# Optimization experiments

Measured on AMD Instinct MI355X. Metric: run time of the kernel, lower is better.

The kernel has to match this reference:

```python
import jax, jax.numpy as jnp
import numpy as np

N_NODES = 100000
N_EDGES = 1600000
IN_DIM = 128
HIDDEN = 128
EPS = 1e-5  # BatchNorm1d default eps


def gcn_conv(x, src, dst, W, b, n_nodes):
    """PyG GCNConv with default add_self_loops=True, edge_weight=None.
    out = D^{-1/2} (A + I) D^{-1/2} X W + b, deg computed from dst (col)."""
    xw = x @ W  # [N, out_dim] -- transform before propagate, as in PyG
    ones = jnp.ones((src.shape[0],), dtype=x.dtype)
    deg = jax.ops.segment_sum(ones, dst, num_segments=n_nodes) + 1.0  # +1 self-loop
    dis = jax.lax.rsqrt(deg)  # deg >= 1 always
    norm = dis[src] * dis[dst]  # [E]
    msgs = xw[src] * norm[:, None]  # [E, out_dim] gather (irregular access)
    agg = jax.ops.segment_sum(msgs, dst, num_segments=n_nodes)
    agg = agg + xw * (1.0 / deg)[:, None]  # self-loop contribution, norm = 1/deg_i
    return agg + b


def batch_norm(x, gamma, beta):
    # training-mode BatchNorm1d: biased batch statistics over the node dim
    m = jnp.mean(x, axis=0)
    v = jnp.mean(jnp.square(x - m), axis=0)
    return gamma * (x - m) * jax.lax.rsqrt(v + EPS) + beta


def setup_inputs() -> dict:
    key = jax.random.key(0)
    ks = jax.random.split(key, 6)
    x = jax.random.normal(ks[0], (N_NODES, IN_DIM), dtype=jnp.float32)
    edge_index = jax.random.randint(ks[1], (2, N_EDGES), 0, N_NODES, dtype=jnp.int64)
    # Glorot-ish scaled weights
    W1 = jax.random.normal(ks[2], (IN_DIM, HIDDEN), dtype=jnp.float32) / np.sqrt(IN_DIM)
    W2 = jax.random.normal(ks[3], (HIDDEN, HIDDEN // 2), dtype=jnp.float32) / np.sqrt(HIDDEN)
    Wf = jax.random.normal(ks[4], (HIDDEN // 2, 1), dtype=jnp.float32) / np.sqrt(HIDDEN // 2)
    return {
        "x": x,
        "edge_index": edge_index,
        "W1": W1, "b1": jnp.zeros((HIDDEN,), jnp.float32),
        "g1": jnp.ones((HIDDEN,), jnp.float32), "beta1": jnp.zeros((HIDDEN,), jnp.float32),
        "W2": W2, "b2": jnp.zeros((HIDDEN // 2,), jnp.float32),
        "g2": jnp.ones((HIDDEN // 2,), jnp.float32), "beta2": jnp.zeros((HIDDEN // 2,), jnp.float32),
        "Wf": Wf, "bf": jnp.zeros((1,), jnp.float32),
    }


def reference(x, edge_index, W1, b1, g1, beta1, W2, b2, g2, beta2, Wf, bf):
    src, dst = edge_index[0], edge_index[1]
    n = x.shape[0]
    h = jax.nn.relu(batch_norm(gcn_conv(x, src, dst, W1, b1, n), g1, beta1))
    # dropout is identity in eval / correctness-baseline mode
    h = jax.nn.relu(batch_norm(gcn_conv(h, src, dst, W2, b2, n), g2, beta2))
    return h @ Wf + bf  # [N, 1]
```

## Files before the change

### kernel.cpp

```cpp
#include <hip/hip_runtime.h>

#define NN 100000
#define NE 1600000
#define D1 128
#define D2 64
#define BN_EPS 1e-5f
#define SCAN_CHUNK 512
#define NB_SCAN ((NN + SCAN_CHUNK - 1) / SCAN_CHUNK)

typedef unsigned int uint32;
typedef unsigned short ushort;
typedef __attribute__((ext_vector_type(8))) short bf16x8;
typedef __attribute__((ext_vector_type(4))) float f32x4;

__device__ __forceinline__ ushort f2bf1(float f) {
    uint32 u = __float_as_uint(f);
    return (ushort)((u + 0x7FFFu + ((u >> 16) & 1u)) >> 16);
}
__device__ __forceinline__ uint32 f2bf_pair(float a, float b) {
    uint32 ua = __float_as_uint(a), ub = __float_as_uint(b);
    ua = (ua + 0x7FFFu + ((ua >> 16) & 1u)) >> 16;
    ub = (ub + 0x7FFFu + ((ub >> 16) & 1u)) >> 16;
    return ua | (ub << 16);
}
__device__ __forceinline__ float bf_lo(uint32 v) { return __uint_as_float(v << 16); }
__device__ __forceinline__ float bf_hi(uint32 v) { return __uint_as_float(v & 0xFFFF0000u); }

__global__ __launch_bounds__(256) void cnt_k(const int* __restrict__ dst,
                                             int* __restrict__ cnt) {
    int i = blockIdx.x * 256 + threadIdx.x;
    if (i < NE) atomicAdd(&cnt[dst[i]], 1);
}

__global__ __launch_bounds__(SCAN_CHUNK) void scan1_k(const int* __restrict__ cnt,
                                                      int* __restrict__ rowptr,
                                                      int* __restrict__ bsum,
                                                      float* __restrict__ dis) {
    __shared__ int sh[SCAN_CHUNK];
    int tid = threadIdx.x;
    int g = blockIdx.x * SCAN_CHUNK + tid;
    int v = (g < NN) ? cnt[g] : 0;
    if (g < NN) dis[g] = rsqrtf((float)v + 1.0f);
    sh[tid] = v;
    __syncthreads();
    for (int o = 1; o < SCAN_CHUNK; o <<= 1) {
        int t = (tid >= o) ? sh[tid - o] : 0;
        __syncthreads();
        sh[tid] += t;
        __syncthreads();
    }
    if (g < NN) rowptr[g] = sh[tid] - v;
    if (tid == SCAN_CHUNK - 1) bsum[blockIdx.x] = sh[tid];
}

__global__ void scan2_k(int* __restrict__ bsum) {
    if (threadIdx.x == 0 && blockIdx.x == 0) {
        int a = 0;
        for (int i = 0; i < NB_SCAN; ++i) { int t = bsum[i]; bsum[i] = a; a += t; }
    }
}

__global__ __launch_bounds__(256) void scan3_k(int* __restrict__ rowptr,
                                               const int* __restrict__ bsum) {
    int g = blockIdx.x * 256 + threadIdx.x;
    if (g < NN) rowptr[g] += bsum[g >> 9];
    if (g == 0) rowptr[NN] = NE;
}

__global__ __launch_bounds__(256) void fill_k(const int* __restrict__ src,
                                              const int* __restrict__ dst,
                                              const int* __restrict__ rowptr,
                                              const float* __restrict__ dis,
                                              int* __restrict__ cur,
                                              int* __restrict__ esrc,
                                              float* __restrict__ ew) {
    int e = blockIdx.x * 256 + threadIdx.x;
    if (e >= NE) return;
    int d = dst[e];
    int s = src[e];
    int p = rowptr[d] + atomicAdd(&cur[d], 1);
    esrc[p] = s;
    ew[p] = dis[s] * dis[d];
}

__global__ __launch_bounds__(256) void wt_k(const float* __restrict__ W1,
                                            const float* __restrict__ W2,
                                            ushort* __restrict__ wt1,
                                            ushort* __restrict__ wt2) {
    int i = blockIdx.x * 256 + threadIdx.x;
    if (i < 128 * 128) {
        int c = i >> 7, k = i & 127;
        wt1[i] = f2bf1(W1[k * 128 + c]);
    } else if (i < 128 * 128 + 64 * 128) {
        int o = i - 128 * 128;
        int c = o >> 7, k = o & 127;
        wt2[o] = f2bf1(W2[k * 64 + c]);
    }
}

__global__ __launch_bounds__(256) void mgemm1_k(const float* __restrict__ X,
                                                const ushort* __restrict__ Wt,
                                                ushort* __restrict__ Yb) {
    const int lane = threadIdx.x & 63;
    const int wv = threadIdx.x >> 6;
    const int row0 = blockIdx.x * 64 + wv * 16;
    const int m = lane & 15;
    const int kg = lane >> 4;
    const int rowA = min(row0 + m, NN - 1);
    f32x4 acc[8];
    #pragma unroll
    for (int t = 0; t < 8; ++t) acc[t] = (f32x4){0.f, 0.f, 0.f, 0.f};

    #pragma unroll
    for (int kc = 0; kc < 128; kc += 32) {
        const int k0 = kc + kg * 8;
        float4 xa = *(const float4*)(X + (size_t)rowA * 128 + k0);
        float4 xb = *(const float4*)(X + (size_t)rowA * 128 + k0 + 4);
        bf16x8 af;
        af[0] = (short)f2bf1(xa.x); af[1] = (short)f2bf1(xa.y);
        af[2] = (short)f2bf1(xa.z); af[3] = (short)f2bf1(xa.w);
        af[4] = (short)f2bf1(xb.x); af[5] = (short)f2bf1(xb.y);
        af[6] = (short)f2bf1(xb.z); af[7] = (short)f2bf1(xb.w);
        #pragma unroll
        for (int t = 0; t < 8; ++t) {
            bf16x8 bfr = *(const bf16x8*)(Wt + (size_t)(t * 16 + m) * 128 + k0);
            acc[t] = __builtin_amdgcn_mfma_f32_16x16x32_bf16(af, bfr, acc[t], 0, 0, 0);
        }
    }
    #pragma unroll
    for (int t = 0; t < 8; ++t)
        #pragma unroll
        for (int r = 0; r < 4; ++r) {
            int rr = row0 + kg * 4 + r;
            if (rr < NN) Yb[(size_t)rr * 128 + t * 16 + m] = f2bf1(acc[t][r]);
        }
}

__global__ __launch_bounds__(256) void mgemm2_k(const ushort* __restrict__ Xb,
                                                const ushort* __restrict__ Wt,
                                                const float* __restrict__ sums,
                                                const float* __restrict__ ssq,
                                                const float* __restrict__ g,
                                                const float* __restrict__ beta,
                                                ushort* __restrict__ Yb) {
    __shared__ float sc[128], shf[128];
    {
        int t = threadIdx.x;
        if (t < 128) {
            float m = sums[t] * (1.0f / NN);
            float var = ssq[t] * (1.0f / NN) - m * m;
            float s = g[t] * rsqrtf(var + BN_EPS);
            sc[t] = s;
            shf[t] = beta[t] - m * s;
        }
    }
    __syncthreads();
    const int lane = threadIdx.x & 63;
    const int wv = threadIdx.x >> 6;
    const int row0 = blockIdx.x * 64 + wv * 16;
    const int m = lane & 15;
    const int kg = lane >> 4;
    const int rowA = min(row0 + m, NN - 1);
    f32x4 acc[4];
    #pragma unroll
    for (int t = 0; t < 4; ++t) acc[t] = (f32x4){0.f, 0.f, 0.f, 0.f};

    #pragma unroll
    for (int kc = 0; kc < 128; kc += 32) {
        const int k0 = kc + kg * 8;
        uint4 raw = *(const uint4*)(Xb + (size_t)rowA * 128 + k0);
        float xs[8];
        xs[0] = bf_lo(raw.x); xs[1] = bf_hi(raw.x);
        xs[2] = bf_lo(raw.y); xs[3] = bf_hi(raw.y);
        xs[4] = bf_lo(raw.z); xs[5] = bf_hi(raw.z);
        xs[6] = bf_lo(raw.w); xs[7] = bf_hi(raw.w);
        float4 sa = *(const float4*)&sc[k0];
        float4 sb = *(const float4*)&sc[k0 + 4];
        float4 ha = *(const float4*)&shf[k0];
        float4 hb = *(const float4*)&shf[k0 + 4];
        xs[0] = fmaxf(fmaf(xs[0], sa.x, ha.x), 0.f);
        xs[1] = fmaxf(fmaf(xs[1], sa.y, ha.y), 0.f);
        xs[2] = fmaxf(fmaf(xs[2], sa.z, ha.z), 0.f);
        xs[3] = fmaxf(fmaf(xs[3], sa.w, ha.w), 0.f);
        xs[4] = fmaxf(fmaf(xs[4], sb.x, hb.x), 0.f);
        xs[5] = fmaxf(fmaf(xs[5], sb.y, hb.y), 0.f);
        xs[6] = fmaxf(fmaf(xs[6], sb.z, hb.z), 0.f);
        xs[7] = fmaxf(fmaf(xs[7], sb.w, hb.w), 0.f);
        bf16x8 af;
        #pragma unroll
        for (int i = 0; i < 8; ++i) af[i] = (short)f2bf1(xs[i]);
        #pragma unroll
        for (int t = 0; t < 4; ++t) {
            bf16x8 bfr = *(const bf16x8*)(Wt + (size_t)(t * 16 + m) * 128 + k0);
            acc[t] = __builtin_amdgcn_mfma_f32_16x16x32_bf16(af, bfr, acc[t], 0, 0, 0);
        }
    }
    #pragma unroll
    for (int t = 0; t < 4; ++t)
        #pragma unroll
        for (int r = 0; r < 4; ++r) {
            int rr = row0 + kg * 4 + r;
            if (rr < NN) Yb[(size_t)rr * 64 + t * 16 + m] = f2bf1(acc[t][r]);
        }
}

__global__ __launch_bounds__(256) void agg128_k(const int* __restrict__ rowptr,
                                                const int* __restrict__ esrc,
                                                const float* __restrict__ ew,
                                                const float* __restrict__ dis,
                                                const uint32* __restrict__ xwb,
                                                const float* __restrict__ b,
                                                uint32* __restrict__ agg1b,
                                                float* __restrict__ sums,
                                                float* __restrict__ ssq) {
    const int lane = threadIdx.x & 63;
    const int wid = (blockIdx.x * 256 + threadIdx.x) >> 6;
    const int nwaves = gridDim.x * 4;
    float s0 = 0.f, s1 = 0.f, q0 = 0.f, q1 = 0.f;
    const float bc0 = b[lane * 2], bc1 = b[lane * 2 + 1];

    for (int n = wid; n < NN; n += nwaves) {
        const int beg = rowptr[n], end = rowptr[n + 1];
        const float dn = dis[n];
        float ax = 0.f, ay = 0.f;
        int e = beg;
        for (; e + 8 <= end; e += 8) {
            int idx[8]; float w[8]; uint32 vv[8];
            #pragma unroll
            for (int j = 0; j < 8; ++j) idx[j] = esrc[e + j];
            #pragma unroll
            for (int j = 0; j < 8; ++j) w[j] = ew[e + j];
            #pragma unroll
            for (int j = 0; j < 8; ++j)
                vv[j] = xwb[(size_t)idx[j] * 64 + lane];
            #pragma unroll
            for (int j = 0; j < 8; ++j) {
                ax = fmaf(bf_lo(vv[j]), w[j], ax);
                ay = fmaf(bf_hi(vv[j]), w[j], ay);
            }
        }
        for (; e < end; ++e) {
            int s = esrc[e];
            float w = ew[e];
            uint32 v = xwb[(size_t)s * 64 + lane];
            ax = fmaf(bf_lo(v), w, ax);
            ay = fmaf(bf_hi(v), w, ay);
        }
        float sl = dn * dn;
        uint32 xv = xwb[(size_t)n * 64 + lane];
        ax = fmaf(bf_lo(xv), sl, ax) + bc0;
        ay = fmaf(bf_hi(xv), sl, ay) + bc1;
        agg1b[(size_t)n * 64 + lane] = f2bf_pair(ax, ay);
        s0 += ax; q0 = fmaf(ax, ax, q0);
        s1 += ay; q1 = fmaf(ay, ay, q1);
    }

    __shared__ float ls[256];
    ls[threadIdx.x] = 0.f;
    __syncthreads();
    atomicAdd(&ls[lane * 2], s0);
    atomicAdd(&ls[lane * 2 + 1], s1);
    atomicAdd(&ls[128 + lane * 2], q0);
    atomicAdd(&ls[128 + lane * 2 + 1], q1);
    __syncthreads();
    if (threadIdx.x < 128) atomicAdd(&sums[threadIdx.x], ls[threadIdx.x]);
    else atomicAdd(&ssq[threadIdx.x - 128], ls[threadIdx.x]);
}

__global__ __launch_bounds__(256) void agg64_k(const int* __restrict__ rowptr,
                                               const int* __restrict__ esrc,
                                               const float* __restrict__ ew,
                                               const float* __restrict__ dis,
                                               const uint32* __restrict__ xwb,
                                               const float* __restrict__ b,
                                               uint32* __restrict__ agg2b,
                                               float* __restrict__ sums,
                                               float* __restrict__ ssq) {
    const int lane = threadIdx.x & 63;
    const int half = lane >> 5;
    const int sl = lane & 31;
    const int wid = (blockIdx.x * 256 + threadIdx.x) >> 6;
    const int nwaves = gridDim.x * 4;
    float s0 = 0.f, s1 = 0.f, q0 = 0.f, q1 = 0.f;
    const float bc0 = b[sl * 2], bc1 = b[sl * 2 + 1];

    for (int n = wid; n < NN; n += nwaves) {
        const int beg = rowptr[n], end = rowptr[n + 1];
        const float dn = dis[n];
        float ax = 0.f, ay = 0.f;
        int e = beg;
        for (; e + 16 <= end; e += 16) {
            int idx[8]; float w[8]; uint32 vv[8];
            #pragma unroll
            for (int j = 0; j < 8; ++j) idx[j] = esrc[e + 2 * j + half];
            #pragma unroll
            for (int j = 0; j < 8; ++j) w[j] = ew[e + 2 * j + half];
            #pragma unroll
            for (int j = 0; j < 8; ++j)
                vv[j] = xwb[(size_t)idx[j] * 32 + sl];
            #pragma unroll
            for (int j = 0; j < 8; ++j) {
                ax = fmaf(bf_lo(vv[j]), w[j], ax);
                ay = fmaf(bf_hi(vv[j]), w[j], ay);
            }
        }
        for (; e + 2 <= end; e += 2) {
            int s = esrc[e + half];
            float w = ew[e + half];
            uint32 v = xwb[(size_t)s * 32 + sl];
            ax = fmaf(bf_lo(v), w, ax);
            ay = fmaf(bf_hi(v), w, ay);
        }
        if (e < end && half == 0) {
            int s = esrc[e];
            float w = ew[e];
            uint32 v = xwb[(size_t)s * 32 + sl];
            ax = fmaf(bf_lo(v), w, ax);
            ay = fmaf(bf_hi(v), w, ay);
        }
        ax += __shfl_down(ax, 32);
        ay += __shfl_down(ay, 32);
        if (half == 0) {
            float slf = dn * dn;
            uint32 xv = xwb[(size_t)n * 32 + sl];
            ax = fmaf(bf_lo(xv), slf, ax) + bc0;
            ay = fmaf(bf_hi(xv), slf, ay) + bc1;
            agg2b[(size_t)n * 32 + sl] = f2bf_pair(ax, ay);
            s0 += ax; q0 = fmaf(ax, ax, q0);
            s1 += ay; q1 = fmaf(ay, ay, q1);
        }
    }

    __shared__ float ls[128];
    if (threadIdx.x < 128) ls[threadIdx.x] = 0.f;
    __syncthreads();
    if (half == 0) {
        atomicAdd(&ls[sl * 2], s0);
        atomicAdd(&ls[sl * 2 + 1], s1);
        atomicAdd(&ls[64 + sl * 2], q0);
        atomicAdd(&ls[64 + sl * 2 + 1], q1);
    }
    __syncthreads();
    if (threadIdx.x < 64) atomicAdd(&sums[threadIdx.x], ls[threadIdx.x]);
    else if (threadIdx.x < 128) atomicAdd(&ssq[threadIdx.x - 64], ls[threadIdx.x]);
}

__global__ __launch_bounds__(256) void final_k(const uint32* __restrict__ h2b,
                                               const float* __restrict__ sums,
                                               const float* __restrict__ ssq,
                                               const float* __restrict__ g,
                                               const float* __restrict__ beta,
                                               const float* __restrict__ Wf,
                                               const float* __restrict__ bf,
                                               float* __restrict__ out) {
    __shared__ float sc[64], shf[64];
    {
        int t = threadIdx.x;
        if (t < 64) {
            float m = sums[t] * (1.0f / NN);
            float var = ssq[t] * (1.0f / NN) - m * m;
            float s = g[t] * rsqrtf(var + BN_EPS);
            sc[t] = s;
            shf[t] = beta[t] - m * s;
        }
    }
    __syncthreads();
    const int lane = threadIdx.x & 63;
    const int half = lane >> 5;
    const int sl = lane & 31;
    const int node = ((blockIdx.x * 256 + threadIdx.x) >> 6) * 2 + half;
    if (node >= NN) return;
    uint32 p = h2b[(size_t)node * 32 + sl];
    float2 wf = *(const float2*)&Wf[sl * 2];
    float v = fmaxf(fmaf(bf_lo(p), sc[sl * 2], shf[sl * 2]), 0.f) * wf.x;
    v = fmaf(fmaxf(fmaf(bf_hi(p), sc[sl * 2 + 1], shf[sl * 2 + 1]), 0.f), wf.y, v);
    #pragma unroll
    for (int o = 16; o > 0; o >>= 1) v += __shfl_down(v, o, 32);
    if (sl == 0) out[node] = v + bf[0];
}

extern "C" void kernel_launch(void* const* d_in, const int* in_sizes, int n_in,
                              void* d_out, int out_size, void* d_ws, size_t ws_size,
                              hipStream_t stream) {
    const float* x   = (const float*)d_in[0];
    const int*   ei  = (const int*)d_in[1];
    const int*   src = ei;
    const int*   dst = ei + NE;
    const float* W1  = (const float*)d_in[2];
    const float* b1  = (const float*)d_in[3];
    const float* g1  = (const float*)d_in[4];
    const float* be1 = (const float*)d_in[5];
    const float* W2  = (const float*)d_in[6];
    const float* b2  = (const float*)d_in[7];
    const float* g2  = (const float*)d_in[8];
    const float* be2 = (const float*)d_in[9];
    const float* Wf  = (const float*)d_in[10];
    const float* bf  = (const float*)d_in[11];
    float* out = (float*)d_out;

    uint32* xwb   = (uint32*)d_ws;
    uint32* agg1b = xwb + (size_t)NN * 64;
    uint32* agg2b = agg1b + (size_t)NN * 64;
    float*  dis   = (float*)(agg2b + (size_t)NN * 32);
    ushort* wt1   = (ushort*)(dis + NN);
    ushort* wt2   = wt1 + 128 * 128;
    int*    rowptr = (int*)(wt2 + 64 * 128);
    int*    bsum   = rowptr + NN + 1;
    int*    esrc   = bsum + 256;
    float*  ew     = (float*)(esrc + NE);
    int*    cnt    = (int*)(ew + NE);
    int*    cur    = cnt + NN;
    float*  sums1  = (float*)(cur + NN);
    float*  ssq1   = sums1 + D1;
    float*  sums2  = ssq1 + D1;
    float*  ssq2   = sums2 + D2;

    hipMemsetAsync(cnt, 0, sizeof(int) * (2 * NN + 2 * D1 + 2 * D2), stream);

    cnt_k<<<(NE + 255) / 256, 256, 0, stream>>>(dst, cnt);
    scan1_k<<<NB_SCAN, SCAN_CHUNK, 0, stream>>>(cnt, rowptr, bsum, dis);
    scan2_k<<<1, 64, 0, stream>>>(bsum);
    scan3_k<<<(NN + 255) / 256, 256, 0, stream>>>(rowptr, bsum);
    fill_k<<<(NE + 255) / 256, 256, 0, stream>>>(src, dst, rowptr, dis, cur, esrc, ew);
    wt_k<<<(128 * 128 + 64 * 128 + 255) / 256, 256, 0, stream>>>(W1, W2, wt1, wt2);

    mgemm1_k<<<(NN + 63) / 64, 256, 0, stream>>>(x, wt1, (ushort*)xwb);
    agg128_k<<<2048, 256, 0, stream>>>(rowptr, esrc, ew, dis, xwb, b1, agg1b, sums1, ssq1);

    mgemm2_k<<<(NN + 63) / 64, 256, 0, stream>>>((const ushort*)agg1b, wt2, sums1, ssq1,
                                                 g1, be1, (ushort*)xwb);
    agg64_k<<<2048, 256, 0, stream>>>(rowptr, esrc, ew, dis, xwb, b2, agg2b, sums2, ssq2);

    final_k<<<(NN / 2 + 3) / 4, 256, 0, stream>>>(agg2b, sums2, ssq2, g2, be2, Wf, bf, out);
}
```

Before: 472.7 us.

## Fuse CSR fill with first GEMM and merge scan phases into one kernel

Merges the serial single-thread block-sum scan and the offset-add into one kernel in which every block redoes a small shared-memory scan of the block sums. Combines the CSR fill and the first bf16 MFMA GEMM into one launch with disjoint block ranges, so the atomic-heavy fill overlaps the compute-bound GEMM. Count and fill now handle two edges per thread using int2 loads, and the weight conversion is moved ahead of the count. This cuts launch count and idle gaps between small kernels, at the cost of redundant per-block scan work and an assumption that NE divides evenly by 512.

```diff
diff --git a/kernel.cpp b/kernel.cpp
--- a/kernel.cpp
+++ b/kernel.cpp
@@ -7,6 +7,8 @@
 #define BN_EPS 1e-5f
 #define SCAN_CHUNK 512
 #define NB_SCAN ((NN + SCAN_CHUNK - 1) / SCAN_CHUNK)
+#define NB_FILL (NE / 512)
+#define NB_G1   ((NN + 63) / 64)
 
 typedef unsigned int uint32;
 typedef unsigned short ushort;
@@ -29,7 +31,9 @@
 __global__ __launch_bounds__(256) void cnt_k(const int* __restrict__ dst,
                                              int* __restrict__ cnt) {
     int i = blockIdx.x * 256 + threadIdx.x;
-    if (i < NE) atomicAdd(&cnt[dst[i]], 1);
+    int2 dd = *(const int2*)&dst[2 * i];
+    atomicAdd(&cnt[dd.x], 1);
+    atomicAdd(&cnt[dd.y], 1);
 }
 
 __global__ __launch_bounds__(SCAN_CHUNK) void scan1_k(const int* __restrict__ cnt,
@@ -53,57 +57,53 @@
     if (tid == SCAN_CHUNK - 1) bsum[blockIdx.x] = sh[tid];
 }
 
-__global__ void scan2_k(int* __restrict__ bsum) {
-    if (threadIdx.x == 0 && blockIdx.x == 0) {
-        int a = 0;
-        for (int i = 0; i < NB_SCAN; ++i) { int t = bsum[i]; bsum[i] = a; a += t; }
-    }
-}
-
-__global__ __launch_bounds__(256) void scan3_k(int* __restrict__ rowptr,
-                                               const int* __restrict__ bsum) {
-    int g = blockIdx.x * 256 + threadIdx.x;
-    if (g < NN) rowptr[g] += bsum[g >> 9];
+__global__ __launch_bounds__(256) void scan23_k(int* __restrict__ rowptr,
+                                                const int* __restrict__ bsum) {
+    __shared__ int bs[256];
+    int tid = threadIdx.x;
+    bs[tid] = (tid < NB_SCAN) ? bsum[tid] : 0;
+    __syncthreads();
+    for (int o = 1; o < 256; o <<= 1) {
+        int t = (tid >= o) ? bs[tid - o] : 0;
+        __syncthreads();
+        bs[tid] += t;
+        __syncthreads();
+    }
+    int g = blockIdx.x * 256 + tid;
+    if (g < NN) {
+        int chunk = g >> 9;
+        int add = (chunk == 0) ? 0 : bs[chunk - 1];
+        rowptr[g] += add;
+    }
     if (g == 0) rowptr[NN] = NE;
 }
 
-__global__ __launch_bounds__(256) void fill_k(const int* __restrict__ src,
-                                              const int* __restrict__ dst,
-                                              const int* __restrict__ rowptr,
-                                              const float* __restrict__ dis,
-                                              int* __restrict__ cur,
-                                              int* __restrict__ esrc,
-                                              float* __restrict__ ew) {
-    int e = blockIdx.x * 256 + threadIdx.x;
-    if (e >= NE) return;
-    int d = dst[e];
-    int s = src[e];
-    int p = rowptr[d] + atomicAdd(&cur[d], 1);
-    esrc[p] = s;
-    ew[p] = dis[s] * dis[d];
-}
-
-__global__ __launch_bounds__(256) void wt_k(const float* __restrict__ W1,
-                                            const float* __restrict__ W2,
-                                            ushort* __restrict__ wt1,
-                                            ushort* __restrict__ wt2) {
-    int i = blockIdx.x * 256 + threadIdx.x;
-    if (i < 128 * 128) {
-        int c = i >> 7, k = i & 127;
-        wt1[i] = f2bf1(W1[k * 128 + c]);
-    } else if (i < 128 * 128 + 64 * 128) {
-        int o = i - 128 * 128;
-        int c = o >> 7, k = o & 127;
-        wt2[o] = f2bf1(W2[k * 64 + c]);
-    }
-}
-
-__global__ __launch_bounds__(256) void mgemm1_k(const float* __restrict__ X,
-                                                const ushort* __restrict__ Wt,
-                                                ushort* __restrict__ Yb) {
+__global__ __launch_bounds__(256) void fillgemm_k(const int* __restrict__ src,
+                                                  const int* __restrict__ dst,
+                                                  const int* __restrict__ rowptr,
+                                                  const float* __restrict__ dis,
+                                                  int* __restrict__ cur,
+                                                  int* __restrict__ esrc,
+                                                  float* __restrict__ ew,
+                                                  const float* __restrict__ X,
+                                                  const ushort* __restrict__ Wt,
+                                                  ushort* __restrict__ Yb) {
+    if (blockIdx.x < NB_FILL) {
+        int i = blockIdx.x * 256 + threadIdx.x;
+        int2 ss = *(const int2*)&src[2 * i];
+        int2 dd = *(const int2*)&dst[2 * i];
+        int p0 = rowptr[dd.x] + atomicAdd(&cur[dd.x], 1);
+        esrc[p0] = ss.x;
+        ew[p0] = dis[ss.x] * dis[dd.x];
+        int p1 = rowptr[dd.y] + atomicAdd(&cur[dd.y], 1);
+        esrc[p1] = ss.y;
+        ew[p1] = dis[ss.y] * dis[dd.y];
+        return;
+    }
+    const int bid = blockIdx.x - NB_FILL;
     const int lane = threadIdx.x & 63;
     const int wv = threadIdx.x >> 6;
-    const int row0 = blockIdx.x * 64 + wv * 16;
+    const int row0 = bid * 64 + wv * 16;
     const int m = lane & 15;
     const int kg = lane >> 4;
     const int rowA = min(row0 + m, NN - 1);
@@ -134,6 +134,21 @@
             int rr = row0 + kg * 4 + r;
             if (rr < NN) Yb[(size_t)rr * 128 + t * 16 + m] = f2bf1(acc[t][r]);
         }
+}
+
+__global__ __launch_bounds__(256) void wt_k(const float* __restrict__ W1,
+                                            const float* __restrict__ W2,
+                                            ushort* __restrict__ wt1,
+                                            ushort* __restrict__ wt2) {
+    int i = blockIdx.x * 256 + threadIdx.x;
+    if (i < 128 * 128) {
+        int c = i >> 7, k = i & 127;
+        wt1[i] = f2bf1(W1[k * 128 + c]);
+    } else if (i < 128 * 128 + 64 * 128) {
+        int o = i - 128 * 128;
+        int c = o >> 7, k = o & 127;
+        wt2[o] = f2bf1(W2[k * 64 + c]);
+    }
 }
 
 __global__ __launch_bounds__(256) void mgemm2_k(const ushort* __restrict__ Xb,
@@ -417,14 +432,14 @@
 
     hipMemsetAsync(cnt, 0, sizeof(int) * (2 * NN + 2 * D1 + 2 * D2), stream);
 
-    cnt_k<<<(NE + 255) / 256, 256, 0, stream>>>(dst, cnt);
+    wt_k<<<(128 * 128 + 64 * 128 + 255) / 256, 256, 0, stream>>>(W1, W2, wt1, wt2);
+    cnt_k<<<NE / 512, 256, 0, stream>>>(dst, cnt);
     scan1_k<<<NB_SCAN, SCAN_CHUNK, 0, stream>>>(cnt, rowptr, bsum, dis);
-    scan2_k<<<1, 64, 0, stream>>>(bsum);
-    scan3_k<<<(NN + 255) / 256, 256, 0, stream>>>(rowptr, bsum);
-    fill_k<<<(NE + 255) / 256, 256, 0, stream>>>(src, dst, rowptr, dis, cur, esrc, ew);
-    wt_k<<<(128 * 128 + 64 * 128 + 255) / 256, 256, 0, stream>>>(W1, W2, wt1, wt2);
-
-    mgemm1_k<<<(NN + 63) / 64, 256, 0, stream>>>(x, wt1, (ushort*)xwb);
+    scan23_k<<<(NN + 255) / 256, 256, 0, stream>>>(rowptr, bsum);
+
+    fillgemm_k<<<NB_FILL + NB_G1, 256, 0, stream>>>(src, dst, rowptr, dis, cur, esrc, ew,
+                                                    x, wt1, (ushort*)xwb);
+
     agg128_k<<<2048, 256, 0, stream>>>(rowptr, esrc, ew, dis, xwb, b1, agg1b, sums1, ssq1);
 
     mgemm2_k<<<(NN + 63) / 64, 256, 0, stream>>>((const ushort*)agg1b, wt2, sums1, ssq1,
```

Measured after the change: 466.3 us. Within noise of the previous version (-1.4%).
